# Performance work log

Hardware: AMD Instinct MI355X
Metric: run time of the kernel (lower is better)

Reference implementation:

```python
import jax, jax.numpy as jnp
import numpy as np

NSAMPLE = 64
RADIUS = 0.05
HMIN = -0.02
HMAX_LIST = (0.01, 0.02, 0.03, 0.04)
BN_EPS = 1e-5
MLP_DIMS = (3, 64, 128, 256)


def setup_inputs() -> dict:
    key = jax.random.key(0)
    ks = jax.random.split(key, 16)
    B, S, N = 2, 1024, 20000
    # points and seeds in a [0,0.5]^3 box so 0.05-radius cylinders are non-empty
    seed_xyz = jax.random.uniform(ks[0], (B, S, 3), dtype=jnp.float32) * 0.5
    pointcloud = jax.random.uniform(ks[1], (B, N, 3), dtype=jnp.float32) * 0.5
    m = jax.random.normal(ks[2], (B, S, 3, 3), dtype=jnp.float32)
    vp_rot, _ = jnp.linalg.qr(m)  # proper-ish random rotations per seed
    inp = {"seed_xyz": seed_xyz, "pointcloud": pointcloud, "vp_rot": vp_rot}
    for i in range(3):
        cin, cout = MLP_DIMS[i], MLP_DIMS[i + 1]
        inp[f"w{i+1}"] = jax.random.normal(ks[3 + i], (cout, cin), dtype=jnp.float32) * (1.0 / np.sqrt(cin))
        inp[f"gamma{i+1}"] = 1.0 + 0.1 * jax.random.normal(ks[6 + i], (cout,), dtype=jnp.float32)
        inp[f"beta{i+1}"] = 0.1 * jax.random.normal(ks[9 + i], (cout,), dtype=jnp.float32)
        inp[f"mean{i+1}"] = 0.1 * jax.random.normal(ks[12 + i], (cout,), dtype=jnp.float32)
        inp[f"var{i+1}"] = jax.random.uniform(ks[15], (cout,), minval=0.5, maxval=1.5, dtype=jnp.float32)
    return inp


def _cylinder_group(rel_rot, hmax):
    # rel_rot: (B, S, N, 3) point coords relative to each seed, in the seed (approach) frame.
    # Cylinder axis = x (approach vector): keep points with hmin < x < hmax and y^2+z^2 < r^2.
    N = rel_rot.shape[2]
    x, y, z = rel_rot[..., 0], rel_rot[..., 1], rel_rot[..., 2]
    mask = (y * y + z * z < RADIUS * RADIUS) & (x > HMIN) & (x < hmax)  # (B,S,N)
    # first NSAMPLE valid indices (ascending), padded with the first valid index (0 if none)
    score = jnp.where(mask, jnp.arange(N, dtype=jnp.int32), N)
    neg_vals, _ = jax.lax.top_k(-score, NSAMPLE)
    idx = -neg_vals  # (B,S,NSAMPLE), value N marks missing
    first = jnp.where(idx[..., :1] >= N, 0, idx[..., :1])
    idx = jnp.where(idx >= N, first, idx)
    return jnp.take_along_axis(rel_rot, idx[..., None], axis=2)  # (B,S,NSAMPLE,3)


def _bn_relu(h, gamma, beta, mean, var):
    inv = gamma / jnp.sqrt(var + BN_EPS)
    s = inv[None, :, None, None]
    b = (beta - mean * inv)[None, :, None, None]
    return jax.nn.relu(h * s + b)


def _forward(seed_xyz, pointcloud, vp_rot, layers):
    B, S, _ = seed_xyz.shape
    D = len(HMAX_LIST)
    rel = pointcloud[:, None, :, :] - seed_xyz[:, :, None, :]        # (B,S,N,3)
    rel_rot = jnp.einsum('bsnc,bscd->bsnd', rel, vp_rot)             # rotate into seed frame (rel @ rot)
    grouped = jnp.stack([_cylinder_group(rel_rot, h) for h in HMAX_LIST], axis=2)  # (B,S,D,ns,3)
    feat = jnp.transpose(grouped, (0, 4, 1, 2, 3)).reshape(B, 3, S * D, NSAMPLE)   # (B,3,S*D,ns)
    for (w, g, be, m, v) in layers:
        feat = _bn_relu(jnp.einsum('oc,bcpn->bopn', w, feat), g, be, m, v)
    vp = jnp.max(feat, axis=-1)                                       # max-pool over nsample
    return vp.reshape(B, -1, S, D)                                    # (B,256,S,D)


def reference(seed_xyz, pointcloud, vp_rot,
              w1, gamma1, beta1, mean1, var1,
              w2, gamma2, beta2, mean2, var2,
              w3, gamma3, beta3, mean3, var3):
    layers = [(w1, gamma1, beta1, mean1, var1),
              (w2, gamma2, beta2, mean2, var2),
              (w3, gamma3, beta3, mean3, var3)]
    return _forward(seed_xyz, pointcloud, vp_rot, layers)
```

## Files before the change

kernel.cpp:

```cpp
#include <hip/hip_runtime.h>

#define NPTS   20000
#define NCHUNK 313

typedef __bf16 bf16x8 __attribute__((ext_vector_type(8)));
typedef float  f32x4  __attribute__((ext_vector_type(4)));

__device__ __forceinline__ unsigned short f2b(float f) {
    __bf16 h = (__bf16)f;
    union { __bf16 h; unsigned short s; } u; u.h = h; return u.s;
}
__device__ __forceinline__ unsigned int pk2(float a, float b) {
    return (unsigned int)f2b(a) | ((unsigned int)f2b(b) << 16);
}

#define WS_BINNED    0
#define WS_PARTHIST  640000
#define WS_COUNTS    721920
#define WS_OFFSETS   726016
#define WS_FLAGS     730112
#define WS_W2P       730368
#define WS_W3P       746752
#define WS_W1E       812288
#define WS_B1E       813056
#define WS_B2E       813312
#define WS_B3E       813824

__global__ __launch_bounds__(512)
void hist_prepack_kernel(const float* __restrict__ pointcloud,
                const float* __restrict__ w1,
                const float* __restrict__ g1,  const float* __restrict__ be1,
                const float* __restrict__ mn1, const float* __restrict__ vr1,
                const float* __restrict__ w2,
                const float* __restrict__ g2,  const float* __restrict__ be2,
                const float* __restrict__ mn2, const float* __restrict__ vr2,
                const float* __restrict__ w3,
                const float* __restrict__ g3,  const float* __restrict__ be3,
                const float* __restrict__ mn3, const float* __restrict__ vr3,
                unsigned int* __restrict__ parthist,
                unsigned short* __restrict__ w2p,
                unsigned short* __restrict__ w3p,
                float* __restrict__ w1e_g, float* __restrict__ b1e_g,
                float* __restrict__ b2e_g, float* __restrict__ b3e_g)
{
    __shared__ unsigned int h[512];
    const int blk = blockIdx.x;
    const int b   = blk / 20;
    const int p   = blk % 20;
    const int tid = threadIdx.x;
    const int gid = blk * 512 + tid;

    for (int e = gid; e < 8192; e += 20480) {
        int row = e >> 6;
        float inv = g2[row] / sqrtf(vr2[row] + 1e-5f);
        w2p[e] = f2b(w2[e] * inv);
    }
    for (int e = gid; e < 32768; e += 20480) {
        int row = e >> 7;
        float inv = g3[row] / sqrtf(vr3[row] + 1e-5f);
        w3p[e] = f2b(w3[e] * inv);
    }
    if (gid < 64) {
        float inv = g1[gid] / sqrtf(vr1[gid] + 1e-5f);
        w1e_g[gid*3+0] = inv * w1[gid*3+0];
        w1e_g[gid*3+1] = inv * w1[gid*3+1];
        w1e_g[gid*3+2] = inv * w1[gid*3+2];
        b1e_g[gid]     = be1[gid] - mn1[gid] * inv;
    }
    if (gid < 128) {
        float inv = g2[gid] / sqrtf(vr2[gid] + 1e-5f);
        b2e_g[gid] = be2[gid] - mn2[gid] * inv;
    }
    if (gid < 256) {
        float inv = g3[gid] / sqrtf(vr3[gid] + 1e-5f);
        b3e_g[gid] = be3[gid] - mn3[gid] * inv;
    }

    h[tid] = 0;
    __syncthreads();

    const float* base = pointcloud + (b * NPTS + p * 1000) * 3;
    for (int i = tid; i < 1000; i += 512) {
        float x = base[i*3+0], y = base[i*3+1], z = base[i*3+2];
        int cx = min(7, (int)(x * 16.0f));
        int cy = min(7, (int)(y * 16.0f));
        int cz = min(7, (int)(z * 16.0f));
        atomicAdd(&h[(cz * 8 + cy) * 8 + cx], 1u);
    }
    __syncthreads();

    parthist[blk * 512 + tid] = h[tid];
}

__global__ __launch_bounds__(512)
void scatter_kernel(const float* __restrict__ pointcloud,
                    const unsigned int* __restrict__ parthist,
                    unsigned int* __restrict__ counts,
                    unsigned int* __restrict__ offsets,
                    float4* __restrict__ binned)
{
    __shared__ unsigned int scanv[512];
    __shared__ unsigned int cur[512];
    const int blk = blockIdx.x;
    const int b   = blk / 20;
    const int p   = blk % 20;
    const int tid = threadIdx.x;

    unsigned int cnt = 0, partial = 0;
    #pragma unroll
    for (int pp = 0; pp < 20; ++pp) {
        unsigned int v = parthist[(b * 20 + pp) * 512 + tid];
        cnt += v;
        if (pp < p) partial += v;
    }
    scanv[tid] = cnt;
    __syncthreads();
    #pragma unroll
    for (int off = 1; off < 512; off <<= 1) {
        unsigned int v = 0;
        if (tid >= off) v = scanv[tid - off];
        __syncthreads();
        scanv[tid] += v;
        __syncthreads();
    }
    unsigned int excl = scanv[tid] - cnt;
    if (p == 0) {
        counts [b * 512 + tid] = cnt;
        offsets[b * 512 + tid] = b * NPTS + excl;
    }
    cur[tid] = b * NPTS + excl + partial;
    __syncthreads();

    const float* base = pointcloud + (b * NPTS + p * 1000) * 3;
    for (int i = tid; i < 1000; i += 512) {
        float x = base[i*3+0], y = base[i*3+1], z = base[i*3+2];
        int cx = min(7, (int)(x * 16.0f));
        int cy = min(7, (int)(y * 16.0f));
        int cz = min(7, (int)(z * 16.0f));
        int cid = (cz * 8 + cy) * 8 + cx;
        unsigned int slot = atomicAdd(&cur[cid], 1u);
        binned[slot] = make_float4(x, y, z, __int_as_float(p * 1000 + i));
    }
}

struct __align__(16) SMemF {
    union {
        struct {
            unsigned int bm[4][640];
            int cstart[64];
            int ccnt[64];
        } a;
        struct {
            unsigned short h1[64][72];
            unsigned short h2[64][136];
        } b;
    } u;
    int    idxs[4][64];
    float  w1e[64][3];
    float  b1e[64];
};

__global__ __launch_bounds__(256, 3)
void fused_kernel(const float* __restrict__ seed_xyz,
                  const float* __restrict__ pointcloud,
                  const float* __restrict__ vp_rot,
                  const unsigned int* __restrict__ counts,
                  const unsigned int* __restrict__ offsets,
                  const float4* __restrict__ binned,
                  const unsigned short* __restrict__ w2p,
                  const unsigned short* __restrict__ w3p,
                  const float* __restrict__ w1e_g, const float* __restrict__ b1e_g,
                  const float* __restrict__ b2e_g, const float* __restrict__ b3e_g,
                  float* __restrict__ out)
{
    __shared__ SMemF sm;
    const int tid = threadIdx.x;
    const int wv  = tid >> 6;
    const int ln  = tid & 63;
    const int q   = ln >> 4;
    const int l15 = ln & 15;

    const int blk = blockIdx.x;
    const int i8  = blk >> 3;
    const int s   = (blk & 7) * 128 + (i8 & 127);
    const int b   = i8 >> 7;
    const int bs  = b * 1024 + s;

    if (tid < 64) {
        sm.w1e[tid][0] = w1e_g[tid*3+0];
        sm.w1e[tid][1] = w1e_g[tid*3+1];
        sm.w1e[tid][2] = w1e_g[tid*3+2];
        sm.b1e[tid]    = b1e_g[tid];
    }

    {
        unsigned int* bmp = &sm.u.a.bm[0][0];
        #pragma unroll
        for (int i = 0; i < 10; ++i) bmp[tid + i * 256] = 0;
    }

    const float sx = seed_xyz[bs*3+0];
    const float sy = seed_xyz[bs*3+1];
    const float sz = seed_xyz[bs*3+2];
    const float R00 = vp_rot[bs*9+0], R01 = vp_rot[bs*9+1], R02 = vp_rot[bs*9+2];
    const float R10 = vp_rot[bs*9+3], R11 = vp_rot[bs*9+4], R12 = vp_rot[bs*9+5];
    const float R20 = vp_rot[bs*9+6], R21 = vp_rot[bs*9+7], R22 = vp_rot[bs*9+8];

    const int lx = max(0, (int)floorf((sx - 0.066f) * 16.f));
    const int hx = min(7, (int)floorf((sx + 0.066f) * 16.f));
    const int ly = max(0, (int)floorf((sy - 0.066f) * 16.f));
    const int hy = min(7, (int)floorf((sy + 0.066f) * 16.f));
    const int lz = max(0, (int)floorf((sz - 0.066f) * 16.f));
    const int hz = min(7, (int)floorf((sz + 0.066f) * 16.f));
    const int nx = hx - lx + 1, ny = hy - ly + 1, nz = hz - lz + 1;
    const int ncell = nx * ny * nz;

    if (tid < ncell) {
        int cz = lz + tid / (nx * ny);
        int rem = tid % (nx * ny);
        int cy = ly + rem / nx;
        int cx = lx + rem % nx;
        int cid = (cz * 8 + cy) * 8 + cx;
        sm.u.a.cstart[tid] = (int)offsets[b * 512 + cid];
        sm.u.a.ccnt[tid]   = (int)counts [b * 512 + cid];
    }
    __syncthreads();

    {
        #pragma clang fp contract(off)
        for (int k = wv; k < ncell; k += 4) {
            const int base = sm.u.a.cstart[k];
            const int cnt  = sm.u.a.ccnt[k];
            for (int i = ln; i < cnt; i += 64) {
                float4 pt = binned[base + i];
                float rx = pt.x - sx, ry = pt.y - sy, rz = pt.z - sz;
                float x = (rx*R00 + ry*R10) + rz*R20;
                float y = (rx*R01 + ry*R11) + rz*R21;
                float z = (rx*R02 + ry*R12) + rz*R22;
                if (((y*y + z*z) < 0.0025f) && (x > -0.02f) && (x < 0.04f)) {
                    int n = __float_as_int(pt.w);
                    unsigned int bit = 1u << (n & 31);
                    int wi = n >> 5;
                    if (x < 0.01f) atomicOr(&sm.u.a.bm[0][wi], bit);
                    if (x < 0.02f) atomicOr(&sm.u.a.bm[1][wi], bit);
                    if (x < 0.03f) atomicOr(&sm.u.a.bm[2][wi], bit);
                    atomicOr(&sm.u.a.bm[3][wi], bit);
                }
            }
        }
    }
    __syncthreads();

    {
        const int d = wv;
        int carry = 0;
        for (int r = 0; r < 5 && carry < 64; ++r) {
            int c = r*64 + ln;
            unsigned long long w = 0ULL;
            if (c < NCHUNK)
                w = ((unsigned long long)sm.u.a.bm[d][2*c+1] << 32)
                  |  (unsigned long long)sm.u.a.bm[d][2*c];
            int wc = __popcll(w);
            int incl = wc;
            #pragma unroll
            for (int off = 1; off < 64; off <<= 1) {
                int t = __shfl_up(incl, off);
                if (ln >= off) incl += t;
            }
            int rank  = carry + incl - wc;
            int total = __shfl(incl, 63);
            while (w && rank < 64) {
                int bp = __builtin_ctzll(w);
                w &= w - 1;
                sm.idxs[d][rank] = c*64 + bp;
                ++rank;
            }
            carry += total;
        }
        int cnt = carry < 64 ? carry : 64;
        int first = (cnt > 0) ? sm.idxs[d][0] : 0;
        if (ln >= cnt) sm.idxs[d][ln] = first;
    }

    __syncthreads();

    auto l1_compute = [&](float p0, float p1, float p2) {
        float x0, x1, x2;
        {
            #pragma clang fp contract(off)
            float rx = p0 - sx, ry = p1 - sy, rz = p2 - sz;
            x0 = (rx*R00 + ry*R10) + rz*R20;
            x1 = (rx*R01 + ry*R11) + rz*R21;
            x2 = (rx*R02 + ry*R12) + rz*R22;
        }
        unsigned int pk[8];
        #pragma unroll
        for (int i = 0; i < 8; ++i) {
            int ch = wv*16 + i*2;
            float ha = fmaf(x0, sm.w1e[ch][0],
                       fmaf(x1, sm.w1e[ch][1],
                       fmaf(x2, sm.w1e[ch][2], sm.b1e[ch])));
            float hb = fmaf(x0, sm.w1e[ch+1][0],
                       fmaf(x1, sm.w1e[ch+1][1],
                       fmaf(x2, sm.w1e[ch+1][2], sm.b1e[ch+1])));
            pk[i] = pk2(fmaxf(ha, 0.f), fmaxf(hb, 0.f));
        }
        *(uint4*)&sm.u.b.h1[ln][wv*16 + 0] = make_uint4(pk[0], pk[1], pk[2], pk[3]);
        *(uint4*)&sm.u.b.h1[ln][wv*16 + 8] = make_uint4(pk[4], pk[5], pk[6], pk[7]);
    };

    {
        int n = sm.idxs[0][ln];
        const float* p = pointcloud + (b*NPTS + n)*3;
        l1_compute(p[0], p[1], p[2]);
    }
    __syncthreads();

    for (int d = 0; d < 4; ++d) {
        float px = 0.f, py = 0.f, pz = 0.f;
        if (d < 3) {
            int n = sm.idxs[d+1][ln];
            const float* p = pointcloud + (b*NPTS + n)*3;
            px = p[0]; py = p[1]; pz = p[2];
        }

        {
            #pragma unroll 1
            for (int m = 0; m < 2; ++m) {
                int row = (wv*2+m)*16 + l15;
                bf16x8 a0 = *(const bf16x8*)(w2p + row*64 +  0 + q*8);
                bf16x8 a1 = *(const bf16x8*)(w2p + row*64 + 32 + q*8);
                f32x4 binit2 = *(const f32x4*)&b2e_g[(wv*2+m)*16 + q*4];
                #pragma unroll
                for (int nt = 0; nt < 4; ++nt) {
                    int n = nt*16 + l15;
                    bf16x8 b0 = *(const bf16x8*)&sm.u.b.h1[n][q*8];
                    bf16x8 b1 = *(const bf16x8*)&sm.u.b.h1[n][32 + q*8];
                    f32x4 acc = binit2;
                    acc = __builtin_amdgcn_mfma_f32_16x16x32_bf16(a0, b0, acc, 0, 0, 0);
                    acc = __builtin_amdgcn_mfma_f32_16x16x32_bf16(a1, b1, acc, 0, 0, 0);
                    int ch0 = (wv*2+m)*16 + q*4;
                    uint2 pkk;
                    pkk.x = pk2(fmaxf(acc[0], 0.f), fmaxf(acc[1], 0.f));
                    pkk.y = pk2(fmaxf(acc[2], 0.f), fmaxf(acc[3], 0.f));
                    *(uint2*)&sm.u.b.h2[n][ch0] = pkk;
                }
            }
        }
        __syncthreads();

        {
            #pragma unroll 1
            for (int m = 0; m < 4; ++m) {
                int row = (wv*4+m)*16 + l15;
                bf16x8 a0 = *(const bf16x8*)(w3p + row*128 +  0 + q*8);
                bf16x8 a1 = *(const bf16x8*)(w3p + row*128 + 32 + q*8);
                bf16x8 a2 = *(const bf16x8*)(w3p + row*128 + 64 + q*8);
                bf16x8 a3 = *(const bf16x8*)(w3p + row*128 + 96 + q*8);
                f32x4 binit3 = *(const f32x4*)&b3e_g[(wv*4+m)*16 + q*4];
                float rm[4];
                #pragma unroll
                for (int r = 0; r < 4; ++r) rm[r] = 0.f;
                #pragma unroll
                for (int nt = 0; nt < 4; ++nt) {
                    int n = nt*16 + l15;
                    bf16x8 bb0 = *(const bf16x8*)&sm.u.b.h2[n][ 0 + q*8];
                    bf16x8 bb1 = *(const bf16x8*)&sm.u.b.h2[n][32 + q*8];
                    bf16x8 bb2 = *(const bf16x8*)&sm.u.b.h2[n][64 + q*8];
                    bf16x8 bb3 = *(const bf16x8*)&sm.u.b.h2[n][96 + q*8];
                    f32x4 acc = binit3;
                    acc = __builtin_amdgcn_mfma_f32_16x16x32_bf16(a0, bb0, acc, 0, 0, 0);
                    acc = __builtin_amdgcn_mfma_f32_16x16x32_bf16(a1, bb1, acc, 0, 0, 0);
                    acc = __builtin_amdgcn_mfma_f32_16x16x32_bf16(a2, bb2, acc, 0, 0, 0);
                    acc = __builtin_amdgcn_mfma_f32_16x16x32_bf16(a3, bb3, acc, 0, 0, 0);
                    #pragma unroll
                    for (int r = 0; r < 4; ++r)
                        rm[r] = fmaxf(rm[r], acc[r]);
                }
                #pragma unroll
                for (int r = 0; r < 4; ++r) {
                    float v = rm[r];
                    v = fmaxf(v, __shfl_xor(v, 1));
                    v = fmaxf(v, __shfl_xor(v, 2));
                    v = fmaxf(v, __shfl_xor(v, 4));
                    v = fmaxf(v, __shfl_xor(v, 8));
                    if (l15 == 0) {
                        int ch = (wv*4+m)*16 + q*4 + r;
                        out[((b*256 + ch)*1024 + s)*4 + d] = v;
                    }
                }
            }

            if (d < 3) l1_compute(px, py, pz);
        }
        if (d < 3) __syncthreads();
    }
}

extern "C" void kernel_launch(void* const* d_in, const int* in_sizes, int n_in,
                              void* d_out, int out_size, void* d_ws, size_t ws_size,
                              hipStream_t stream) {
    (void)in_sizes; (void)n_in; (void)out_size; (void)ws_size;
    const float* seed = (const float*)d_in[0];
    const float* pc   = (const float*)d_in[1];
    const float* rot  = (const float*)d_in[2];
    const float* w1   = (const float*)d_in[3];
    const float* g1   = (const float*)d_in[4];
    const float* be1  = (const float*)d_in[5];
    const float* mn1  = (const float*)d_in[6];
    const float* vr1  = (const float*)d_in[7];
    const float* w2   = (const float*)d_in[8];
    const float* g2   = (const float*)d_in[9];
    const float* be2  = (const float*)d_in[10];
    const float* mn2  = (const float*)d_in[11];
    const float* vr2  = (const float*)d_in[12];
    const float* w3   = (const float*)d_in[13];
    const float* g3   = (const float*)d_in[14];
    const float* be3  = (const float*)d_in[15];
    const float* mn3  = (const float*)d_in[16];
    const float* vr3  = (const float*)d_in[17];

    char* ws = (char*)d_ws;
    float4*         binned   = (float4*)(ws + WS_BINNED);
    unsigned int*   parthist = (unsigned int*)(ws + WS_PARTHIST);
    unsigned int*   counts   = (unsigned int*)(ws + WS_COUNTS);
    unsigned int*   offsets  = (unsigned int*)(ws + WS_OFFSETS);
    unsigned short* w2p      = (unsigned short*)(ws + WS_W2P);
    unsigned short* w3p      = (unsigned short*)(ws + WS_W3P);
    float*          w1e_g    = (float*)(ws + WS_W1E);
    float*          b1e_g    = (float*)(ws + WS_B1E);
    float*          b2e_g    = (float*)(ws + WS_B2E);
    float*          b3e_g    = (float*)(ws + WS_B3E);

    hist_prepack_kernel<<<dim3(40), dim3(512), 0, stream>>>(
        pc,
        w1, g1, be1, mn1, vr1,
        w2, g2, be2, mn2, vr2,
        w3, g3, be3, mn3, vr3,
        parthist,
        w2p, w3p, w1e_g, b1e_g, b2e_g, b3e_g);
    scatter_kernel<<<dim3(40), dim3(512), 0, stream>>>(
        pc, parthist, counts, offsets, binned);
    fused_kernel  <<<dim3(2048), dim3(256), 0, stream>>>(
        seed, pc, rot, counts, offsets, binned,
        w2p, w3p, w1e_g, b1e_g, b2e_g, b3e_g,
        (float*)d_out);
}
```

Before: 196.4 us.

## Split fused kernel into separate scan-select and MLP kernels via workspace indices

Splits the single fused kernel into a neighbor scan/select kernel, which writes 64 sample indices per seed and depth as uint16 to workspace, and a separate MLP kernel that reads them back. The scan kernel no longer carries MLP registers and shared memory, so it can run at a higher occupancy hint (6 blocks per CU), which suits the latency-bound gather and atomic phase. The cost is an extra kernel launch, a global round-trip of the index buffer, and losing the overlap between the scan and MLP phases that different blocks had inside one kernel.

```diff
diff --git a/kernel.cpp b/kernel.cpp
--- a/kernel.cpp
+++ b/kernel.cpp
@@ -25,6 +25,7 @@
 #define WS_B1E       813056
 #define WS_B2E       813312
 #define WS_B3E       813824
+#define WS_IDX       814848
 
 __global__ __launch_bounds__(512)
 void hist_prepack_kernel(const float* __restrict__ pointcloud,
@@ -143,42 +144,26 @@
     }
 }
 
-struct __align__(16) SMemF {
-    union {
-        struct {
-            unsigned int bm[4][640];
-            int cstart[64];
-            int ccnt[64];
-        } a;
-        struct {
-            unsigned short h1[64][72];
-            unsigned short h2[64][136];
-        } b;
-    } u;
-    int    idxs[4][64];
-    float  w1e[64][3];
-    float  b1e[64];
+
+struct __align__(16) SMemS {
+    unsigned int bm[4][640];
+    int cstart[64];
+    int ccnt[64];
+    int idxs[4][64];
 };
 
-__global__ __launch_bounds__(256, 3)
-void fused_kernel(const float* __restrict__ seed_xyz,
-                  const float* __restrict__ pointcloud,
-                  const float* __restrict__ vp_rot,
-                  const unsigned int* __restrict__ counts,
-                  const unsigned int* __restrict__ offsets,
-                  const float4* __restrict__ binned,
-                  const unsigned short* __restrict__ w2p,
-                  const unsigned short* __restrict__ w3p,
-                  const float* __restrict__ w1e_g, const float* __restrict__ b1e_g,
-                  const float* __restrict__ b2e_g, const float* __restrict__ b3e_g,
-                  float* __restrict__ out)
+__global__ __launch_bounds__(256, 6)
+void scan_select_kernel(const float* __restrict__ seed_xyz,
+                        const float* __restrict__ vp_rot,
+                        const unsigned int* __restrict__ counts,
+                        const unsigned int* __restrict__ offsets,
+                        const float4* __restrict__ binned,
+                        unsigned short* __restrict__ idx_out)
 {
-    __shared__ SMemF sm;
+    __shared__ SMemS sm;
     const int tid = threadIdx.x;
     const int wv  = tid >> 6;
     const int ln  = tid & 63;
-    const int q   = ln >> 4;
-    const int l15 = ln & 15;
 
     const int blk = blockIdx.x;
     const int i8  = blk >> 3;
@@ -186,15 +171,8 @@
     const int b   = i8 >> 7;
     const int bs  = b * 1024 + s;
 
-    if (tid < 64) {
-        sm.w1e[tid][0] = w1e_g[tid*3+0];
-        sm.w1e[tid][1] = w1e_g[tid*3+1];
-        sm.w1e[tid][2] = w1e_g[tid*3+2];
-        sm.b1e[tid]    = b1e_g[tid];
-    }
-
     {
-        unsigned int* bmp = &sm.u.a.bm[0][0];
+        unsigned int* bmp = &sm.bm[0][0];
         #pragma unroll
         for (int i = 0; i < 10; ++i) bmp[tid + i * 256] = 0;
     }
@@ -221,16 +199,16 @@
         int cy = ly + rem / nx;
         int cx = lx + rem % nx;
         int cid = (cz * 8 + cy) * 8 + cx;
-        sm.u.a.cstart[tid] = (int)offsets[b * 512 + cid];
-        sm.u.a.ccnt[tid]   = (int)counts [b * 512 + cid];
+        sm.cstart[tid] = (int)offsets[b * 512 + cid];
+        sm.ccnt[tid]   = (int)counts [b * 512 + cid];
     }
     __syncthreads();
 
     {
         #pragma clang fp contract(off)
         for (int k = wv; k < ncell; k += 4) {
-            const int base = sm.u.a.cstart[k];
-            const int cnt  = sm.u.a.ccnt[k];
+            const int base = sm.cstart[k];
+            const int cnt  = sm.ccnt[k];
             for (int i = ln; i < cnt; i += 64) {
                 float4 pt = binned[base + i];
                 float rx = pt.x - sx, ry = pt.y - sy, rz = pt.z - sz;
@@ -241,10 +219,10 @@
                     int n = __float_as_int(pt.w);
                     unsigned int bit = 1u << (n & 31);
                     int wi = n >> 5;
-                    if (x < 0.01f) atomicOr(&sm.u.a.bm[0][wi], bit);
-                    if (x < 0.02f) atomicOr(&sm.u.a.bm[1][wi], bit);
-                    if (x < 0.03f) atomicOr(&sm.u.a.bm[2][wi], bit);
-                    atomicOr(&sm.u.a.bm[3][wi], bit);
+                    if (x < 0.01f) atomicOr(&sm.bm[0][wi], bit);
+                    if (x < 0.02f) atomicOr(&sm.bm[1][wi], bit);
+                    if (x < 0.03f) atomicOr(&sm.bm[2][wi], bit);
+                    atomicOr(&sm.bm[3][wi], bit);
                 }
             }
         }
@@ -258,8 +236,8 @@
             int c = r*64 + ln;
             unsigned long long w = 0ULL;
             if (c < NCHUNK)
-                w = ((unsigned long long)sm.u.a.bm[d][2*c+1] << 32)
-                  |  (unsigned long long)sm.u.a.bm[d][2*c];
+                w = ((unsigned long long)sm.bm[d][2*c+1] << 32)
+                  |  (unsigned long long)sm.bm[d][2*c];
             int wc = __popcll(w);
             int incl = wc;
             #pragma unroll
@@ -279,10 +257,55 @@
         }
         int cnt = carry < 64 ? carry : 64;
         int first = (cnt > 0) ? sm.idxs[d][0] : 0;
-        if (ln >= cnt) sm.idxs[d][ln] = first;
-    }
-
-    __syncthreads();
+        int v = (ln < cnt) ? sm.idxs[d][ln] : first;
+        idx_out[(bs*4 + d)*64 + ln] = (unsigned short)v;
+    }
+}
+
+struct __align__(16) SMemM {
+    unsigned short h1[64][72];
+    unsigned short h2[64][136];
+    float w1e[64][3];
+    float b1e[64];
+};
+
+__global__ __launch_bounds__(256, 3)
+void mlp_kernel(const float* __restrict__ seed_xyz,
+                const float* __restrict__ pointcloud,
+                const float* __restrict__ vp_rot,
+                const unsigned short* __restrict__ idx_in,
+                const unsigned short* __restrict__ w2p,
+                const unsigned short* __restrict__ w3p,
+                const float* __restrict__ w1e_g, const float* __restrict__ b1e_g,
+                const float* __restrict__ b2e_g, const float* __restrict__ b3e_g,
+                float* __restrict__ out)
+{
+    __shared__ SMemM sm;
+    const int tid = threadIdx.x;
+    const int wv  = tid >> 6;
+    const int ln  = tid & 63;
+    const int q   = ln >> 4;
+    const int l15 = ln & 15;
+
+    const int blk = blockIdx.x;
+    const int i8  = blk >> 3;
+    const int s   = (blk & 7) * 128 + (i8 & 127);
+    const int b   = i8 >> 7;
+    const int bs  = b * 1024 + s;
+
+    if (tid < 64) {
+        sm.w1e[tid][0] = w1e_g[tid*3+0];
+        sm.w1e[tid][1] = w1e_g[tid*3+1];
+        sm.w1e[tid][2] = w1e_g[tid*3+2];
+        sm.b1e[tid]    = b1e_g[tid];
+    }
+
+    const float sx = seed_xyz[bs*3+0];
+    const float sy = seed_xyz[bs*3+1];
+    const float sz = seed_xyz[bs*3+2];
+    const float R00 = vp_rot[bs*9+0], R01 = vp_rot[bs*9+1], R02 = vp_rot[bs*9+2];
+    const float R10 = vp_rot[bs*9+3], R11 = vp_rot[bs*9+4], R12 = vp_rot[bs*9+5];
+    const float R20 = vp_rot[bs*9+6], R21 = vp_rot[bs*9+7], R22 = vp_rot[bs*9+8];
 
     auto l1_compute = [&](float p0, float p1, float p2) {
         float x0, x1, x2;
@@ -305,12 +328,14 @@
                        fmaf(x2, sm.w1e[ch+1][2], sm.b1e[ch+1])));
             pk[i] = pk2(fmaxf(ha, 0.f), fmaxf(hb, 0.f));
         }
-        *(uint4*)&sm.u.b.h1[ln][wv*16 + 0] = make_uint4(pk[0], pk[1], pk[2], pk[3]);
-        *(uint4*)&sm.u.b.h1[ln][wv*16 + 8] = make_uint4(pk[4], pk[5], pk[6], pk[7]);
+        *(uint4*)&sm.h1[ln][wv*16 + 0] = make_uint4(pk[0], pk[1], pk[2], pk[3]);
+        *(uint4*)&sm.h1[ln][wv*16 + 8] = make_uint4(pk[4], pk[5], pk[6], pk[7]);
     };
 
+    __syncthreads();
+
     {
-        int n = sm.idxs[0][ln];
+        int n = (int)idx_in[(bs*4 + 0)*64 + ln];
         const float* p = pointcloud + (b*NPTS + n)*3;
         l1_compute(p[0], p[1], p[2]);
     }
@@ -319,7 +344,7 @@
     for (int d = 0; d < 4; ++d) {
         float px = 0.f, py = 0.f, pz = 0.f;
         if (d < 3) {
-            int n = sm.idxs[d+1][ln];
+            int n = (int)idx_in[(bs*4 + d+1)*64 + ln];
             const float* p = pointcloud + (b*NPTS + n)*3;
             px = p[0]; py = p[1]; pz = p[2];
         }
@@ -334,8 +359,8 @@
                 #pragma unroll
                 for (int nt = 0; nt < 4; ++nt) {
                     int n = nt*16 + l15;
-                    bf16x8 b0 = *(const bf16x8*)&sm.u.b.h1[n][q*8];
-                    bf16x8 b1 = *(const bf16x8*)&sm.u.b.h1[n][32 + q*8];
+                    bf16x8 b0 = *(const bf16x8*)&sm.h1[n][q*8];
+                    bf16x8 b1 = *(const bf16x8*)&sm.h1[n][32 + q*8];
                     f32x4 acc = binit2;
                     acc = __builtin_amdgcn_mfma_f32_16x16x32_bf16(a0, b0, acc, 0, 0, 0);
                     acc = __builtin_amdgcn_mfma_f32_16x16x32_bf16(a1, b1, acc, 0, 0, 0);
@@ -343,7 +368,7 @@
                     uint2 pkk;
                     pkk.x = pk2(fmaxf(acc[0], 0.f), fmaxf(acc[1], 0.f));
                     pkk.y = pk2(fmaxf(acc[2], 0.f), fmaxf(acc[3], 0.f));
-                    *(uint2*)&sm.u.b.h2[n][ch0] = pkk;
+                    *(uint2*)&sm.h2[n][ch0] = pkk;
                 }
             }
         }
@@ -364,10 +389,10 @@
                 #pragma unroll
                 for (int nt = 0; nt < 4; ++nt) {
                     int n = nt*16 + l15;
-                    bf16x8 bb0 = *(const bf16x8*)&sm.u.b.h2[n][ 0 + q*8];
-                    bf16x8 bb1 = *(const bf16x8*)&sm.u.b.h2[n][32 + q*8];
-                    bf16x8 bb2 = *(const bf16x8*)&sm.u.b.h2[n][64 + q*8];
-                    bf16x8 bb3 = *(const bf16x8*)&sm.u.b.h2[n][96 + q*8];
+                    bf16x8 bb0 = *(const bf16x8*)&sm.h2[n][ 0 + q*8];
+                    bf16x8 bb1 = *(const bf16x8*)&sm.h2[n][32 + q*8];
+                    bf16x8 bb2 = *(const bf16x8*)&sm.h2[n][64 + q*8];
+                    bf16x8 bb3 = *(const bf16x8*)&sm.h2[n][96 + q*8];
                     f32x4 acc = binit3;
                     acc = __builtin_amdgcn_mfma_f32_16x16x32_bf16(a0, bb0, acc, 0, 0, 0);
                     acc = __builtin_amdgcn_mfma_f32_16x16x32_bf16(a1, bb1, acc, 0, 0, 0);
@@ -431,6 +456,7 @@
     float*          b1e_g    = (float*)(ws + WS_B1E);
     float*          b2e_g    = (float*)(ws + WS_B2E);
     float*          b3e_g    = (float*)(ws + WS_B3E);
+    unsigned short* idx_ws   = (unsigned short*)(ws + WS_IDX);
 
     hist_prepack_kernel<<<dim3(40), dim3(512), 0, stream>>>(
         pc,
@@ -441,8 +467,10 @@
         w2p, w3p, w1e_g, b1e_g, b2e_g, b3e_g);
     scatter_kernel<<<dim3(40), dim3(512), 0, stream>>>(
         pc, parthist, counts, offsets, binned);
-    fused_kernel  <<<dim3(2048), dim3(256), 0, stream>>>(
-        seed, pc, rot, counts, offsets, binned,
+    scan_select_kernel<<<dim3(2048), dim3(256), 0, stream>>>(
+        seed, rot, counts, offsets, binned, idx_ws);
+    mlp_kernel<<<dim3(2048), dim3(256), 0, stream>>>(
+        seed, pc, rot, idx_ws,
         w2p, w3p, w1e_g, b1e_g, b2e_g, b3e_g,
         (float*)d_out);
 }
```

Measured after the change: 197.4 us. No clear change (+0.5%).
